# Optimization experiments

Hardware: AMD Instinct MI355X
Metric: run time of the kernel (lower is better)

## Reference

```python
import jax, jax.numpy as jnp
import numpy as np

N_ORDER = 256
BATCH = 512
SEQ_LEN = 4096


def make_legs_matrices(N):
    # HiPPO-LegS: A[n,k] = -sqrt(2n+1)sqrt(2k+1) for n>k, -(n+1) for n==k, 0 for n<k
    # B[n] = sqrt(2n+1)
    q = np.arange(N, dtype=np.float64)
    r = np.sqrt(2.0 * q + 1.0)
    M = r[:, None] * r[None, :] * (q[:, None] > q[None, :]).astype(np.float64)
    M = M + np.diag(q + 1.0)
    A = -M
    B = r[:, None]
    return jnp.asarray(A, jnp.float32), jnp.asarray(B, jnp.float32)


def setup_inputs() -> dict:
    key = jax.random.key(0)
    A, Bm = make_legs_matrices(N_ORDER)
    f = jax.random.normal(key, (BATCH, SEQ_LEN), dtype=jnp.float32)
    init_state = jnp.zeros((BATCH, 1, N_ORDER), dtype=jnp.float32)
    return {"f": f, "A": A, "Bm": Bm, "init_state": init_state}


def reference(f, A, Bm, init_state):
    # Generalized bilinear transform discretization, alpha = 0.5, step = 1.0
    step = 1.0
    alpha = 0.5
    N = A.shape[0]
    I = jnp.eye(N, dtype=A.dtype)
    inv_step = 1.0 / step
    part1 = I - inv_step * alpha * A
    part2 = I + inv_step * (1.0 - alpha) * A
    # Original uses lstsq; part1 is nonsingular so solve is equivalent.
    Ad = jnp.linalg.solve(part1, part2)            # (N, N)
    Bd = jnp.linalg.solve(part1, inv_step * Bm)    # (N, 1)

    BdT = Bd.T[None]  # (1, 1, N)

    def step_fn(c, f_k):
        # c: (B, 1, N), f_k: (B,)
        # c_k = c_{k-1} @ Ad^T + Bd^T * f_k
        c = jnp.einsum('bin,mn->bim', c, Ad) + BdT * f_k[:, None, None]
        return c, None

    # scan over time axis; batch fully vectorized inside each step
    c_k, _ = jax.lax.scan(step_fn, init_state, jnp.swapaxes(f, 0, 1))
    return c_k  # (B, 1, N)
```

## Files before the change

### kernel.cpp

```cpp
#include <hip/hip_runtime.h>

#define NORD 256
#define TLEN 4096
#define HTLEN 2048
#define NBATCH 512


__device__ __forceinline__ void tile_fma4(const float (*As)[68], const float (*Bs)[68],
                                          int tr, int tc, float acc[4][4]) {
#pragma unroll
  for (int k = 0; k < 32; ++k) {
    const float4 a4 = *reinterpret_cast<const float4*>(&As[k][4 * tr]);
    const float4 b4 = *reinterpret_cast<const float4*>(&Bs[k][4 * tc]);
    const float a[4] = {a4.x, a4.y, a4.z, a4.w};
    const float b[4] = {b4.x, b4.y, b4.z, b4.w};
#pragma unroll
    for (int ii = 0; ii < 4; ++ii)
#pragma unroll
      for (int jj = 0; jj < 4; ++jj)
        acc[ii][jj] += a[ii] * b[jj];
  }
}

__device__ __forceinline__ void fill_tr(float (*dst)[68], const float* __restrict__ s0,
                                        const float* __restrict__ s1,
                                        int row0, int stride, int k0, int t) {
  const int rr = t >> 3, cc = (t & 7) << 2;
#pragma unroll
  for (int p = 0; p < 64; p += 32) {
    const size_t off = (size_t)(row0 + rr + p) * stride + k0 + cc;
    float4 v = *reinterpret_cast<const float4*>(s0 + off);
    if (s1) {
      const float4 w = *reinterpret_cast<const float4*>(s1 + off);
      v.x += w.x; v.y += w.y; v.z += w.z; v.w += w.w;
    }
    dst[cc + 0][rr + p] = v.x; dst[cc + 1][rr + p] = v.y;
    dst[cc + 2][rr + p] = v.z; dst[cc + 3][rr + p] = v.w;
  }
}

__global__ __launch_bounds__(256) void k_inv(const float* __restrict__ A,
                                             const float* __restrict__ Bm,
                                             float* __restrict__ P00, float* P01,
                                             float* __restrict__ U0, float* U1) {
  const int bid = blockIdx.x;
  const int i = threadIdx.x;
  const int wave = i >> 6, lane = i & 63;
  __shared__ float xs[NORD];
  float b = (bid < NORD) ? ((i == bid) ? 1.0f : 0.0f) : Bm[i];
  const float invd = 1.0f / (1.0f - 0.5f * A[i * NORD + i]);
  for (int w = 0; w < 4; ++w) {
    if (wave == w) {
      const int base = w << 6;
      for (int jj = 0; jj < 64; ++jj) {
        float bj = __shfl(b, jj);
        float dj = __shfl(invd, jj);
        float xj = bj * dj;
        if (lane > jj) {
          b += 0.5f * A[i * NORD + base + jj] * xj;
        } else if (lane == jj) {
          b = xj;
        }
      }
      xs[i] = b;
    }
    __syncthreads();
    if (wave > w) {
      const int base = w << 6;
      const float4* arow = reinterpret_cast<const float4*>(A + i * NORD + base);
#pragma unroll
      for (int q = 0; q < 16; ++q) {
        float4 a4 = arow[q];
        b += 0.5f * (a4.x * xs[base + 4 * q + 0] + a4.y * xs[base + 4 * q + 1] +
                     a4.z * xs[base + 4 * q + 2] + a4.w * xs[base + 4 * q + 3]);
      }
    }
  }
  if (bid < NORD) {
    P00[i * NORD + bid] = 2.0f * b - ((i == bid) ? 1.0f : 0.0f);
    if (P01) P01[(size_t)bid * 256 + i] = 0.0f;
  } else {
    U0[i] = b;
    if (U1) U1[i] = 0.0f;
  }
}

__global__ __launch_bounds__(256) void k_stage(float* U0, float* U1,
                                               const float* Pin0, const float* Pin1,
                                               float* Pout0, float* Pout1,
                                               int J, int n_apply) {
  const int bid = blockIdx.x;
  const int t = threadIdx.x;
  const int tr = t >> 4, tc = t & 15;
  __shared__ float As[32][68];
  __shared__ float Bs[32][68];
  const int kspan = U1 ? 128 : 256;

  if (bid < n_apply) {
    int work = bid, ks = 0;
    if (U1) { ks = work & 1; work >>= 1; }
    const int j0 = (work >> 2) << 6;
    const int m0 = (work & 3) << 6;
    const int klo = ks * kspan;
    float acc[4][4] = {};
    for (int kc = 0; kc < kspan; kc += 32) {
      const int k0 = klo + kc;
      fill_tr(As, U0, U1, j0, NORD, k0, t);
      fill_tr(Bs, Pin0, Pin1, m0, NORD, k0, t);
      __syncthreads();
      tile_fma4(As, Bs, tr, tc, acc);
      __syncthreads();
    }
    float* Ud = ks ? U1 : U0;
#pragma unroll
    for (int ii = 0; ii < 4; ++ii) {
      const int lr = j0 + 4 * tr + ii;
      if (lr < J) {
        float4 v = {acc[ii][0], acc[ii][1], acc[ii][2], acc[ii][3]};
        *reinterpret_cast<float4*>(&Ud[(size_t)(J + lr) * NORD + m0 + 4 * tc]) = v;
      }
    }
  } else {
    int q = bid - n_apply, ks = 0;
    if (Pin1) { ks = q & 1; q >>= 1; }
    const int m0s = (q >> 2) << 6;
    const int n0 = (q & 3) << 6;
    const int klo = ks * kspan;
    const int rr = t >> 3, cc = (t & 7) << 2;
    float acc[4][4] = {};
    for (int kc = 0; kc < kspan; kc += 32) {
      const int k0 = klo + kc;
      fill_tr(As, Pin0, Pin1, m0s, NORD, k0, t);
#pragma unroll
      for (int p = 0; p < 64; p += 32) {
        const size_t off = (size_t)(k0 + rr) * NORD + n0 + cc + p;
        float4 v = *reinterpret_cast<const float4*>(Pin0 + off);
        if (Pin1) {
          const float4 w = *reinterpret_cast<const float4*>(Pin1 + off);
          v.x += w.x; v.y += w.y; v.z += w.z; v.w += w.w;
        }
        *reinterpret_cast<float4*>(&Bs[rr][cc + p]) = v;
      }
      __syncthreads();
      tile_fma4(As, Bs, tr, tc, acc);
      __syncthreads();
    }
    float* Pd = ks ? Pout1 : Pout0;
#pragma unroll
    for (int ii = 0; ii < 4; ++ii) {
      float4 v = {acc[ii][0], acc[ii][1], acc[ii][2], acc[ii][3]};
      *reinterpret_cast<float4*>(&Pd[(size_t)(m0s + 4 * tr + ii) * NORD + n0 + 4 * tc]) = v;
    }
  }
}

__global__ __launch_bounds__(256) void k_final(const float* __restrict__ f,
                                               const float* __restrict__ U0,
                                               const float* U1,
                                               float* __restrict__ Glow,
                                               float* __restrict__ C) {
  const int bid = blockIdx.x;
  const int tile = bid & 31, ksf = bid >> 5;
  const int rt = tile >> 1, ct = tile & 1;
  const int h = rt >> 3;
  const int b0 = (rt & 7) << 6;
  const int m0 = ct << 7;
  const int jbase = ksf << 7;
  const int t = threadIdx.x;
  const int tr = t >> 4, tc = t & 15;
  __shared__ float As[32][68];
  __shared__ float Bs0[32][68];
  __shared__ float Bs1[32][68];
  const int rr = t >> 3, cc = (t & 7) << 2;
  const int jr = t >> 5, c32 = t & 31;
  float acc[4][8] = {};
  for (int kc = 0; kc < 128; kc += 32) {
    const int j0 = jbase + kc;
#pragma unroll
    for (int p = 0; p < 64; p += 32) {
      const float4 v = *reinterpret_cast<const float4*>(
          f + (size_t)(b0 + rr + p) * TLEN + HTLEN * h + j0 + cc);
      As[cc + 0][rr + p] = v.x; As[cc + 1][rr + p] = v.y;
      As[cc + 2][rr + p] = v.z; As[cc + 3][rr + p] = v.w;
    }
#pragma unroll
    for (int p = 0; p < 32; p += 8) {
      const int jj = jr + p;
      const size_t off = (size_t)(HTLEN - 1 - (j0 + jj)) * NORD + m0 + 4 * c32;
      float4 v = *reinterpret_cast<const float4*>(U0 + off);
      if (U1) {
        const float4 w = *reinterpret_cast<const float4*>(U1 + off);
        v.x += w.x; v.y += w.y; v.z += w.z; v.w += w.w;
      }
      if (c32 < 16) *reinterpret_cast<float4*>(&Bs0[jj][4 * c32]) = v;
      else          *reinterpret_cast<float4*>(&Bs1[jj][4 * (c32 - 16)]) = v;
    }
    __syncthreads();
#pragma unroll
    for (int k = 0; k < 32; ++k) {
      const float4 a4 = *reinterpret_cast<const float4*>(&As[k][4 * tr]);
      const float4 b4 = *reinterpret_cast<const float4*>(&Bs0[k][4 * tc]);
      const float4 b5 = *reinterpret_cast<const float4*>(&Bs1[k][4 * tc]);
      const float a[4] = {a4.x, a4.y, a4.z, a4.w};
      const float b[8] = {b4.x, b4.y, b4.z, b4.w, b5.x, b5.y, b5.z, b5.w};
#pragma unroll
      for (int ii = 0; ii < 4; ++ii)
#pragma unroll
        for (int jj = 0; jj < 8; ++jj)
          acc[ii][jj] += a[ii] * b[jj];
    }
    __syncthreads();
  }
  float* dst = h ? C : Glow;
#pragma unroll
  for (int ii = 0; ii < 4; ++ii) {
    const int row = b0 + 4 * tr + ii;
#pragma unroll
    for (int jj = 0; jj < 8; ++jj) {
      const int col = m0 + ((jj < 4) ? (4 * tc + jj) : (64 + 4 * tc + (jj - 4)));
      atomicAdd(dst + (size_t)row * NORD + col, acc[ii][jj]);
    }
  }
}

__global__ __launch_bounds__(256) void k_combine(const float* __restrict__ Glow,
                                                 const float* __restrict__ P0,
                                                 const float* P1,
                                                 float* __restrict__ C) {
  const int bid = blockIdx.x;
  const int b0 = (bid >> 2) << 6;
  const int m0 = (bid & 3) << 6;
  const int t = threadIdx.x;
  const int tr = t >> 4, tc = t & 15;
  __shared__ float As[32][68];
  __shared__ float Bs[32][68];
  float acc[4][4] = {};
  for (int k0 = 0; k0 < NORD; k0 += 32) {
    fill_tr(As, Glow, nullptr, b0, NORD, k0, t);
    fill_tr(Bs, P0, P1, m0, NORD, k0, t);
    __syncthreads();
    tile_fma4(As, Bs, tr, tc, acc);
    __syncthreads();
  }
#pragma unroll
  for (int ii = 0; ii < 4; ++ii)
#pragma unroll
    for (int jj = 0; jj < 4; ++jj) {
      float* p = C + (size_t)(b0 + 4 * tr + ii) * NORD + m0 + 4 * tc + jj;
      *p += acc[ii][jj];
    }
}

extern "C" void kernel_launch(void* const* d_in, const int* in_sizes, int n_in,
                              void* d_out, int out_size, void* d_ws, size_t ws_size,
                              hipStream_t stream) {
  const float* f  = (const float*)d_in[0];
  const float* A  = (const float*)d_in[1];
  const float* Bm = (const float*)d_in[2];

  float* ws = (float*)d_ws;
  const size_t need_split = (size_t)(4 * 65536 + 2 * 524288 + 131072) * sizeof(float);
  const int KS = (ws_size >= need_split) ? 2 : 1;

  float *P00, *P01, *P10, *P11, *U0, *U1, *Glow;
  if (KS == 2) {
    P00 = ws;            P01 = ws + 65536;
    P10 = ws + 131072;   P11 = ws + 196608;
    U0  = ws + 262144;   U1  = U0 + 524288;
    Glow = U0 + 1048576;
  } else {
    P00 = ws;            P01 = nullptr;
    P10 = ws + 65536;    P11 = nullptr;
    U0  = ws + 131072;   U1  = nullptr;
    Glow = ws + 655360;
  }
  float* C = (float*)d_out;

  hipMemsetAsync(d_out, 0, (size_t)NBATCH * NORD * sizeof(float), stream);
  hipMemsetAsync(Glow, 0, (size_t)NBATCH * NORD * sizeof(float), stream);

  hipLaunchKernelGGL(k_inv, dim3(NORD + 1), dim3(256), 0, stream, A, Bm, P00, P01, U0, U1);

  for (int s = 0; s <= 10; ++s) {
    const int J = 1 << s;
    const float* Pin0 = (s & 1) ? P10 : P00;
    const float* Pin1 = (s & 1) ? P11 : P01;
    float* Pout0 = (s & 1) ? P00 : P10;
    float* Pout1 = (s & 1) ? P01 : P11;
    const int rtiles = (J + 63) >> 6;
    const int n_apply = (rtiles << 2) * KS;
    const int n_sq = 16 * KS;
    hipLaunchKernelGGL(k_stage, dim3(n_apply + n_sq), dim3(256), 0, stream,
                       U0, U1, Pin0, Pin1, Pout0, Pout1, J, n_apply);
  }

  hipLaunchKernelGGL(k_final, dim3(512), dim3(256), 0, stream, f, U0, U1, Glow, C);
  hipLaunchKernelGGL(k_combine, dim3(32), dim3(256), 0, stream, Glow, P10, P11, C);
}
```

Before: 259.9 us.

## Fuse all stages into one cooperative persistent kernel with hierarchical grid barrier

Replaces the separate inverse, eleven doubling-stage, final and combine launches plus two memsets with a single cooperative kernel of 256 blocks. Phases are separated by a two-level atomic grid barrier, and the memsets are folded into phase 0. The final phase is re-tiled so each block covers a 256-long time chunk instead of 128. The goal is to remove per-launch overhead and idle gaps between the many small launches. In exchange every block pays barrier latency at each phase, and most blocks sit idle during the small stages.

Measured after the change: 456.4 us. +75.6%, slower.

```diff
diff --git a/kernel.cpp b/kernel.cpp
--- a/kernel.cpp
+++ b/kernel.cpp
@@ -4,7 +4,36 @@
 #define TLEN 4096
 #define HTLEN 2048
 #define NBATCH 512
-
+#define NBLK 256
+#define NTHR 256
+
+__device__ __forceinline__ void gbar(int* bar) {
+  __syncthreads();
+  if (threadIdx.x == 0) {
+    int* gen = bar;
+    int* root = bar + 32;
+    int* grpc = bar + 64 + ((blockIdx.x >> 4) << 5);
+    const int g = __hip_atomic_load(gen, __ATOMIC_RELAXED, __HIP_MEMORY_SCOPE_AGENT);
+    __threadfence();
+    bool last = false;
+    if (__hip_atomic_fetch_add(grpc, 1, __ATOMIC_ACQ_REL, __HIP_MEMORY_SCOPE_AGENT) ==
+        (g << 4) + 15) {
+      if (__hip_atomic_fetch_add(root, 1, __ATOMIC_ACQ_REL, __HIP_MEMORY_SCOPE_AGENT) ==
+          (g << 4) + 15) {
+        __hip_atomic_store(gen, g + 1, __ATOMIC_RELEASE, __HIP_MEMORY_SCOPE_AGENT);
+        last = true;
+      }
+    }
+    if (!last) {
+      for (int spin = 0; spin < (1 << 22); ++spin) {
+        if (__hip_atomic_load(gen, __ATOMIC_RELAXED, __HIP_MEMORY_SCOPE_AGENT) != g) break;
+        __builtin_amdgcn_s_sleep(2);
+      }
+    }
+    __threadfence();
+  }
+  __syncthreads();
+}
 
 __device__ __forceinline__ void tile_fma4(const float (*As)[68], const float (*Bs)[68],
                                           int tr, int tc, float acc[4][4]) {
@@ -39,216 +68,227 @@
   }
 }
 
-__global__ __launch_bounds__(256) void k_inv(const float* __restrict__ A,
-                                             const float* __restrict__ Bm,
-                                             float* __restrict__ P00, float* P01,
-                                             float* __restrict__ U0, float* U1) {
-  const int bid = blockIdx.x;
-  const int i = threadIdx.x;
-  const int wave = i >> 6, lane = i & 63;
-  __shared__ float xs[NORD];
-  float b = (bid < NORD) ? ((i == bid) ? 1.0f : 0.0f) : Bm[i];
-  const float invd = 1.0f / (1.0f - 0.5f * A[i * NORD + i]);
-  for (int w = 0; w < 4; ++w) {
-    if (wave == w) {
-      const int base = w << 6;
-      for (int jj = 0; jj < 64; ++jj) {
-        float bj = __shfl(b, jj);
-        float dj = __shfl(invd, jj);
-        float xj = bj * dj;
-        if (lane > jj) {
-          b += 0.5f * A[i * NORD + base + jj] * xj;
-        } else if (lane == jj) {
-          b = xj;
-        }
-      }
-      xs[i] = b;
-    }
-    __syncthreads();
-    if (wave > w) {
-      const int base = w << 6;
-      const float4* arow = reinterpret_cast<const float4*>(A + i * NORD + base);
-#pragma unroll
-      for (int q = 0; q < 16; ++q) {
-        float4 a4 = arow[q];
-        b += 0.5f * (a4.x * xs[base + 4 * q + 0] + a4.y * xs[base + 4 * q + 1] +
-                     a4.z * xs[base + 4 * q + 2] + a4.w * xs[base + 4 * q + 3]);
-      }
-    }
-  }
-  if (bid < NORD) {
-    P00[i * NORD + bid] = 2.0f * b - ((i == bid) ? 1.0f : 0.0f);
-    if (P01) P01[(size_t)bid * 256 + i] = 0.0f;
-  } else {
-    U0[i] = b;
-    if (U1) U1[i] = 0.0f;
-  }
-}
-
-__global__ __launch_bounds__(256) void k_stage(float* U0, float* U1,
-                                               const float* Pin0, const float* Pin1,
-                                               float* Pout0, float* Pout1,
-                                               int J, int n_apply) {
+__global__ __launch_bounds__(NTHR) void hippo_all(
+    const float* __restrict__ A, const float* __restrict__ Bm,
+    const float* __restrict__ f,
+    float* P00, float* P01, float* P10, float* P11,
+    float* U0, float* U1, float* Glow, float* C,
+    int* bar, int ph_lo, int ph_hi, int use_bar) {
   const int bid = blockIdx.x;
   const int t = threadIdx.x;
   const int tr = t >> 4, tc = t & 15;
-  __shared__ float As[32][68];
-  __shared__ float Bs[32][68];
-  const int kspan = U1 ? 128 : 256;
-
-  if (bid < n_apply) {
-    int work = bid, ks = 0;
-    if (U1) { ks = work & 1; work >>= 1; }
-    const int j0 = (work >> 2) << 6;
-    const int m0 = (work & 3) << 6;
-    const int klo = ks * kspan;
-    float acc[4][4] = {};
-    for (int kc = 0; kc < kspan; kc += 32) {
-      const int k0 = klo + kc;
-      fill_tr(As, U0, U1, j0, NORD, k0, t);
-      fill_tr(Bs, Pin0, Pin1, m0, NORD, k0, t);
-      __syncthreads();
-      tile_fma4(As, Bs, tr, tc, acc);
-      __syncthreads();
-    }
-    float* Ud = ks ? U1 : U0;
-#pragma unroll
-    for (int ii = 0; ii < 4; ++ii) {
-      const int lr = j0 + 4 * tr + ii;
-      if (lr < J) {
-        float4 v = {acc[ii][0], acc[ii][1], acc[ii][2], acc[ii][3]};
-        *reinterpret_cast<float4*>(&Ud[(size_t)(J + lr) * NORD + m0 + 4 * tc]) = v;
-      }
-    }
-  } else {
-    int q = bid - n_apply, ks = 0;
-    if (Pin1) { ks = q & 1; q >>= 1; }
-    const int m0s = (q >> 2) << 6;
-    const int n0 = (q & 3) << 6;
-    const int klo = ks * kspan;
-    const int rr = t >> 3, cc = (t & 7) << 2;
-    float acc[4][4] = {};
-    for (int kc = 0; kc < kspan; kc += 32) {
-      const int k0 = klo + kc;
-      fill_tr(As, Pin0, Pin1, m0s, NORD, k0, t);
-#pragma unroll
-      for (int p = 0; p < 64; p += 32) {
-        const size_t off = (size_t)(k0 + rr) * NORD + n0 + cc + p;
-        float4 v = *reinterpret_cast<const float4*>(Pin0 + off);
-        if (Pin1) {
-          const float4 w = *reinterpret_cast<const float4*>(Pin1 + off);
-          v.x += w.x; v.y += w.y; v.z += w.z; v.w += w.w;
-        }
-        *reinterpret_cast<float4*>(&Bs[rr][cc + p]) = v;
-      }
-      __syncthreads();
-      tile_fma4(As, Bs, tr, tc, acc);
-      __syncthreads();
-    }
-    float* Pd = ks ? Pout1 : Pout0;
-#pragma unroll
-    for (int ii = 0; ii < 4; ++ii) {
-      float4 v = {acc[ii][0], acc[ii][1], acc[ii][2], acc[ii][3]};
-      *reinterpret_cast<float4*>(&Pd[(size_t)(m0s + 4 * tr + ii) * NORD + n0 + 4 * tc]) = v;
-    }
-  }
-}
-
-__global__ __launch_bounds__(256) void k_final(const float* __restrict__ f,
-                                               const float* __restrict__ U0,
-                                               const float* U1,
-                                               float* __restrict__ Glow,
-                                               float* __restrict__ C) {
-  const int bid = blockIdx.x;
-  const int tile = bid & 31, ksf = bid >> 5;
-  const int rt = tile >> 1, ct = tile & 1;
-  const int h = rt >> 3;
-  const int b0 = (rt & 7) << 6;
-  const int m0 = ct << 7;
-  const int jbase = ksf << 7;
-  const int t = threadIdx.x;
-  const int tr = t >> 4, tc = t & 15;
+
+  __shared__ float xs[NORD];
   __shared__ float As[32][68];
   __shared__ float Bs0[32][68];
   __shared__ float Bs1[32][68];
-  const int rr = t >> 3, cc = (t & 7) << 2;
-  const int jr = t >> 5, c32 = t & 31;
-  float acc[4][8] = {};
-  for (int kc = 0; kc < 128; kc += 32) {
-    const int j0 = jbase + kc;
-#pragma unroll
-    for (int p = 0; p < 64; p += 32) {
-      const float4 v = *reinterpret_cast<const float4*>(
-          f + (size_t)(b0 + rr + p) * TLEN + HTLEN * h + j0 + cc);
-      As[cc + 0][rr + p] = v.x; As[cc + 1][rr + p] = v.y;
-      As[cc + 2][rr + p] = v.z; As[cc + 3][rr + p] = v.w;
-    }
-#pragma unroll
-    for (int p = 0; p < 32; p += 8) {
-      const int jj = jr + p;
-      const size_t off = (size_t)(HTLEN - 1 - (j0 + jj)) * NORD + m0 + 4 * c32;
-      float4 v = *reinterpret_cast<const float4*>(U0 + off);
-      if (U1) {
-        const float4 w = *reinterpret_cast<const float4*>(U1 + off);
-        v.x += w.x; v.y += w.y; v.z += w.z; v.w += w.w;
-      }
-      if (c32 < 16) *reinterpret_cast<float4*>(&Bs0[jj][4 * c32]) = v;
-      else          *reinterpret_cast<float4*>(&Bs1[jj][4 * (c32 - 16)]) = v;
-    }
-    __syncthreads();
-#pragma unroll
-    for (int k = 0; k < 32; ++k) {
-      const float4 a4 = *reinterpret_cast<const float4*>(&As[k][4 * tr]);
-      const float4 b4 = *reinterpret_cast<const float4*>(&Bs0[k][4 * tc]);
-      const float4 b5 = *reinterpret_cast<const float4*>(&Bs1[k][4 * tc]);
-      const float a[4] = {a4.x, a4.y, a4.z, a4.w};
-      const float b[8] = {b4.x, b4.y, b4.z, b4.w, b5.x, b5.y, b5.z, b5.w};
+
+  for (int ph = ph_lo; ph <= ph_hi; ++ph) {
+    if (ph == 0) {
+      {
+        const int base = bid * 512;
+        C[base + t] = 0.0f; C[base + 256 + t] = 0.0f;
+        Glow[base + t] = 0.0f; Glow[base + 256 + t] = 0.0f;
+        if (P01) P01[(size_t)bid * 256 + t] = 0.0f;
+        if (U1 && bid == 0) U1[t] = 0.0f;
+      }
+      const int ntask = (bid == 0) ? 2 : 1;
+      for (int task = 0; task < ntask; ++task) {
+        const int col = (task == 0) ? (NORD - 1 - bid) : -1;
+        const int i = t;
+        const int wave = i >> 6, lane = i & 63;
+        float b = (col >= 0) ? ((i == col) ? 1.0f : 0.0f) : Bm[i];
+        const float invd = 1.0f / (1.0f - 0.5f * A[i * NORD + i]);
+        for (int w = 0; w < 4; ++w) {
+          if (wave == w) {
+            const int base = w << 6;
+            for (int jj = 0; jj < 64; ++jj) {
+              float bj = __shfl(b, jj);
+              float dj = __shfl(invd, jj);
+              float xj = bj * dj;
+              if (lane > jj) {
+                b += 0.5f * A[i * NORD + base + jj] * xj;
+              } else if (lane == jj) {
+                b = xj;
+              }
+            }
+            xs[i] = b;
+          }
+          __syncthreads();
+          if (wave > w) {
+            const int base = w << 6;
+            const float4* arow = reinterpret_cast<const float4*>(A + i * NORD + base);
+#pragma unroll
+            for (int q = 0; q < 16; ++q) {
+              float4 a4 = arow[q];
+              b += 0.5f * (a4.x * xs[base + 4 * q + 0] + a4.y * xs[base + 4 * q + 1] +
+                           a4.z * xs[base + 4 * q + 2] + a4.w * xs[base + 4 * q + 3]);
+            }
+          }
+        }
+        if (col >= 0) {
+          P00[i * NORD + col] = 2.0f * b - ((i == col) ? 1.0f : 0.0f);
+        } else {
+          U0[i] = b;
+        }
+        __syncthreads();
+      }
+    } else if (ph <= 11) {
+      const int s = ph - 1;
+      const int J = 1 << s;
+      const float* Pin0 = (s & 1) ? P10 : P00;
+      const float* Pin1 = (s & 1) ? P11 : P01;
+      float* Pout0 = (s & 1) ? P00 : P10;
+      float* Pout1 = (s & 1) ? P01 : P11;
+      const int KS = U1 ? 2 : 1;
+      const int rtiles = (J + 63) >> 6;
+      const int n_apply = (rtiles << 2) * KS;
+      const int kspan = U1 ? 128 : 256;
+
+      if (bid < n_apply) {
+        int work = bid, ks = 0;
+        if (U1) { ks = work & 1; work >>= 1; }
+        const int j0 = (work >> 2) << 6;
+        const int m0 = (work & 3) << 6;
+        const int klo = ks * kspan;
+        float acc[4][4] = {};
+        for (int kc = 0; kc < kspan; kc += 32) {
+          const int k0 = klo + kc;
+          fill_tr(As, U0, U1, j0, NORD, k0, t);
+          fill_tr(Bs0, Pin0, Pin1, m0, NORD, k0, t);
+          __syncthreads();
+          tile_fma4(As, Bs0, tr, tc, acc);
+          __syncthreads();
+        }
+        float* Ud = ks ? U1 : U0;
+#pragma unroll
+        for (int ii = 0; ii < 4; ++ii) {
+          const int lr = j0 + 4 * tr + ii;
+          if (lr < J) {
+            float4 v = {acc[ii][0], acc[ii][1], acc[ii][2], acc[ii][3]};
+            *reinterpret_cast<float4*>(&Ud[(size_t)(J + lr) * NORD + m0 + 4 * tc]) = v;
+          }
+        }
+      } else if (bid < n_apply + 16 * KS) {
+        int q = bid - n_apply, ks = 0;
+        if (Pin1) { ks = q & 1; q >>= 1; }
+        const int m0s = (q >> 2) << 6;
+        const int n0 = (q & 3) << 6;
+        const int klo = ks * kspan;
+        const int rr = t >> 3, cc = (t & 7) << 2;
+        float acc[4][4] = {};
+        for (int kc = 0; kc < kspan; kc += 32) {
+          const int k0 = klo + kc;
+          fill_tr(As, Pin0, Pin1, m0s, NORD, k0, t);
+#pragma unroll
+          for (int p = 0; p < 64; p += 32) {
+            const size_t off = (size_t)(k0 + rr) * NORD + n0 + cc + p;
+            float4 v = *reinterpret_cast<const float4*>(Pin0 + off);
+            if (Pin1) {
+              const float4 w = *reinterpret_cast<const float4*>(Pin1 + off);
+              v.x += w.x; v.y += w.y; v.z += w.z; v.w += w.w;
+            }
+            *reinterpret_cast<float4*>(&Bs0[rr][cc + p]) = v;
+          }
+          __syncthreads();
+          tile_fma4(As, Bs0, tr, tc, acc);
+          __syncthreads();
+        }
+        float* Pd = ks ? Pout1 : Pout0;
+#pragma unroll
+        for (int ii = 0; ii < 4; ++ii) {
+          float4 v = {acc[ii][0], acc[ii][1], acc[ii][2], acc[ii][3]};
+          *reinterpret_cast<float4*>(&Pd[(size_t)(m0s + 4 * tr + ii) * NORD + n0 + 4 * tc]) = v;
+        }
+      }
+    } else if (ph == 12) {
+      const int tile = bid >> 3, ks = bid & 7;
+      const int rt = tile >> 1, ct = tile & 1;
+      const int h = rt >> 3;
+      const int b0 = (rt & 7) << 6;
+      const int m0 = ct << 7;
+      const int jbase = ks << 8;
+      const int rr = t >> 3, cc = (t & 7) << 2;
+      const int jr = t >> 5, c32 = t & 31;
+      float acc[4][8] = {};
+      for (int kc = 0; kc < 256; kc += 32) {
+        const int j0 = jbase + kc;
+#pragma unroll
+        for (int p = 0; p < 64; p += 32) {
+          const float4 v = *reinterpret_cast<const float4*>(
+              f + (size_t)(b0 + rr + p) * TLEN + HTLEN * h + j0 + cc);
+          As[cc + 0][rr + p] = v.x; As[cc + 1][rr + p] = v.y;
+          As[cc + 2][rr + p] = v.z; As[cc + 3][rr + p] = v.w;
+        }
+#pragma unroll
+        for (int p = 0; p < 32; p += 8) {
+          const int jj = jr + p;
+          const size_t off = (size_t)(HTLEN - 1 - (j0 + jj)) * NORD + m0 + 4 * c32;
+          float4 v = *reinterpret_cast<const float4*>(U0 + off);
+          if (U1) {
+            const float4 w = *reinterpret_cast<const float4*>(U1 + off);
+            v.x += w.x; v.y += w.y; v.z += w.z; v.w += w.w;
+          }
+          if (c32 < 16) *reinterpret_cast<float4*>(&Bs0[jj][4 * c32]) = v;
+          else          *reinterpret_cast<float4*>(&Bs1[jj][4 * (c32 - 16)]) = v;
+        }
+        __syncthreads();
+#pragma unroll
+        for (int k = 0; k < 32; ++k) {
+          const float4 a4 = *reinterpret_cast<const float4*>(&As[k][4 * tr]);
+          const float4 b4 = *reinterpret_cast<const float4*>(&Bs0[k][4 * tc]);
+          const float4 b5 = *reinterpret_cast<const float4*>(&Bs1[k][4 * tc]);
+          const float a[4] = {a4.x, a4.y, a4.z, a4.w};
+          const float b[8] = {b4.x, b4.y, b4.z, b4.w, b5.x, b5.y, b5.z, b5.w};
+#pragma unroll
+          for (int ii = 0; ii < 4; ++ii)
+#pragma unroll
+            for (int jj = 0; jj < 8; ++jj)
+              acc[ii][jj] += a[ii] * b[jj];
+        }
+        __syncthreads();
+      }
+      float* dst = h ? C : Glow;
+#pragma unroll
+      for (int ii = 0; ii < 4; ++ii) {
+        const int row = b0 + 4 * tr + ii;
+#pragma unroll
+        for (int jj = 0; jj < 8; ++jj) {
+          const int col = m0 + ((jj < 4) ? (4 * tc + jj) : (64 + 4 * tc + (jj - 4)));
+          atomicAdd(dst + (size_t)row * NORD + col, acc[ii][jj]);
+        }
+      }
+    } else if (bid < 32) {
+      const int b0 = (bid >> 2) << 6;
+      const int m0 = (bid & 3) << 6;
+      const int rr = t >> 3, cc = (t & 7) << 2;
+      float acc[4][4] = {};
+      for (int k0 = 0; k0 < NORD; k0 += 32) {
+#pragma unroll
+        for (int p = 0; p < 64; p += 32) {
+          const size_t off = (size_t)(b0 + rr + p) * NORD + k0 + cc;
+#pragma unroll
+          for (int q = 0; q < 4; ++q)
+            As[cc + q][rr + p] =
+                __hip_atomic_load(Glow + off + q, __ATOMIC_RELAXED, __HIP_MEMORY_SCOPE_AGENT);
+        }
+        fill_tr(Bs0, P10, P11, m0, NORD, k0, t);
+        __syncthreads();
+        tile_fma4(As, Bs0, tr, tc, acc);
+        __syncthreads();
+      }
 #pragma unroll
       for (int ii = 0; ii < 4; ++ii)
 #pragma unroll
-        for (int jj = 0; jj < 8; ++jj)
-          acc[ii][jj] += a[ii] * b[jj];
-    }
-    __syncthreads();
-  }
-  float* dst = h ? C : Glow;
-#pragma unroll
-  for (int ii = 0; ii < 4; ++ii) {
-    const int row = b0 + 4 * tr + ii;
-#pragma unroll
-    for (int jj = 0; jj < 8; ++jj) {
-      const int col = m0 + ((jj < 4) ? (4 * tc + jj) : (64 + 4 * tc + (jj - 4)));
-      atomicAdd(dst + (size_t)row * NORD + col, acc[ii][jj]);
-    }
-  }
-}
-
-__global__ __launch_bounds__(256) void k_combine(const float* __restrict__ Glow,
-                                                 const float* __restrict__ P0,
-                                                 const float* P1,
-                                                 float* __restrict__ C) {
-  const int bid = blockIdx.x;
-  const int b0 = (bid >> 2) << 6;
-  const int m0 = (bid & 3) << 6;
-  const int t = threadIdx.x;
-  const int tr = t >> 4, tc = t & 15;
-  __shared__ float As[32][68];
-  __shared__ float Bs[32][68];
-  float acc[4][4] = {};
-  for (int k0 = 0; k0 < NORD; k0 += 32) {
-    fill_tr(As, Glow, nullptr, b0, NORD, k0, t);
-    fill_tr(Bs, P0, P1, m0, NORD, k0, t);
-    __syncthreads();
-    tile_fma4(As, Bs, tr, tc, acc);
-    __syncthreads();
-  }
-#pragma unroll
-  for (int ii = 0; ii < 4; ++ii)
-#pragma unroll
-    for (int jj = 0; jj < 4; ++jj) {
-      float* p = C + (size_t)(b0 + 4 * tr + ii) * NORD + m0 + 4 * tc + jj;
-      *p += acc[ii][jj];
-    }
+        for (int jj = 0; jj < 4; ++jj) {
+          float* p = C + (size_t)(b0 + 4 * tr + ii) * NORD + m0 + 4 * tc + jj;
+          const float cur =
+              __hip_atomic_load(p, __ATOMIC_RELAXED, __HIP_MEMORY_SCOPE_AGENT);
+          *p = cur + acc[ii][jj];
+        }
+    }
+    if (use_bar && ph < ph_hi) gbar(bar);
+  }
 }
 
 extern "C" void kernel_launch(void* const* d_in, const int* in_sizes, int n_in,
@@ -259,41 +299,41 @@
   const float* Bm = (const float*)d_in[2];
 
   float* ws = (float*)d_ws;
-  const size_t need_split = (size_t)(4 * 65536 + 2 * 524288 + 131072) * sizeof(float);
+  const size_t need_split =
+      (size_t)(4 * 65536 + 2 * 524288 + 131072 + 1024) * sizeof(float);
   const int KS = (ws_size >= need_split) ? 2 : 1;
 
   float *P00, *P01, *P10, *P11, *U0, *U1, *Glow;
+  int* bar;
   if (KS == 2) {
     P00 = ws;            P01 = ws + 65536;
     P10 = ws + 131072;   P11 = ws + 196608;
-    U0  = ws + 262144;   U1  = U0 + 524288;
-    Glow = U0 + 1048576;
+    U0  = ws + 262144;   U1  = ws + 786432;
+    Glow = ws + 1310720;
+    bar = (int*)(ws + 1441792);
   } else {
     P00 = ws;            P01 = nullptr;
     P10 = ws + 65536;    P11 = nullptr;
     U0  = ws + 131072;   U1  = nullptr;
     Glow = ws + 655360;
+    bar = (int*)(ws + 786432);
   }
   float* C = (float*)d_out;
 
-  hipMemsetAsync(d_out, 0, (size_t)NBATCH * NORD * sizeof(float), stream);
-  hipMemsetAsync(Glow, 0, (size_t)NBATCH * NORD * sizeof(float), stream);
-
-  hipLaunchKernelGGL(k_inv, dim3(NORD + 1), dim3(256), 0, stream, A, Bm, P00, P01, U0, U1);
-
-  for (int s = 0; s <= 10; ++s) {
-    const int J = 1 << s;
-    const float* Pin0 = (s & 1) ? P10 : P00;
-    const float* Pin1 = (s & 1) ? P11 : P01;
-    float* Pout0 = (s & 1) ? P00 : P10;
-    float* Pout1 = (s & 1) ? P01 : P11;
-    const int rtiles = (J + 63) >> 6;
-    const int n_apply = (rtiles << 2) * KS;
-    const int n_sq = 16 * KS;
-    hipLaunchKernelGGL(k_stage, dim3(n_apply + n_sq), dim3(256), 0, stream,
-                       U0, U1, Pin0, Pin1, Pout0, Pout1, J, n_apply);
-  }
-
-  hipLaunchKernelGGL(k_final, dim3(512), dim3(256), 0, stream, f, U0, U1, Glow, C);
-  hipLaunchKernelGGL(k_combine, dim3(32), dim3(256), 0, stream, Glow, P10, P11, C);
-}
+  hipMemsetAsync(bar, 0, 576 * sizeof(int), stream);
+
+  int pl = 0, phh = 13, ub = 1;
+  void* args[] = {(void*)&A, (void*)&Bm, (void*)&f,
+                  (void*)&P00, (void*)&P01, (void*)&P10, (void*)&P11,
+                  (void*)&U0, (void*)&U1, (void*)&Glow, (void*)&C,
+                  (void*)&bar, (void*)&pl, (void*)&phh, (void*)&ub};
+  hipError_t e = hipLaunchCooperativeKernel((void*)hippo_all, dim3(NBLK), dim3(NTHR),
+                                            args, 0, stream);
+  if (e != hipSuccess) {
+    for (int p = 0; p <= 13; ++p) {
+      hipLaunchKernelGGL(hippo_all, dim3(NBLK), dim3(NTHR), 0, stream,
+                         A, Bm, f, P00, P01, P10, P11, U0, U1, Glow, C,
+                         bar, p, p, 0);
+    }
+  }
+}
```

## Extend impulse-response table to full sequence and drop combine pass

Applied to the files above, without the earlier changes.

Runs one more doubling stage so the Krylov table U covers all 4096 timesteps instead of half. The final state then comes from a single GEMM of f against the reversed U, and the two-half Glow buffer and the k_combine multiply by P are removed. The output zeroing moves into k_inv, replacing the two memsets, and k_final is retiled to 32 batch rows by 256 columns. In exchange, the extra stage doubles U generation work and its memory footprint, and the final GEMM reads twice as much U data.

Result: faster. 246.4 us (-5.2%).

```diff
diff --git a/kernel.cpp b/kernel.cpp
--- a/kernel.cpp
+++ b/kernel.cpp
@@ -2,9 +2,7 @@
 
 #define NORD 256
 #define TLEN 4096
-#define HTLEN 2048
 #define NBATCH 512
-
 
 __device__ __forceinline__ void tile_fma4(const float (*As)[68], const float (*Bs)[68],
                                           int tr, int tc, float acc[4][4]) {
@@ -42,11 +40,17 @@
 __global__ __launch_bounds__(256) void k_inv(const float* __restrict__ A,
                                              const float* __restrict__ Bm,
                                              float* __restrict__ P00, float* P01,
-                                             float* __restrict__ U0, float* U1) {
+                                             float* __restrict__ U0, float* U1,
+                                             float* __restrict__ C) {
   const int bid = blockIdx.x;
   const int i = threadIdx.x;
   const int wave = i >> 6, lane = i & 63;
   __shared__ float xs[NORD];
+  if (bid < NORD) {
+    const int base = bid * 512;
+    C[base + i] = 0.0f;
+    C[base + 256 + i] = 0.0f;
+  }
   float b = (bid < NORD) ? ((i == bid) ? 1.0f : 0.0f) : Bm[i];
   const float invd = 1.0f / (1.0f - 0.5f * A[i * NORD + i]);
   for (int w = 0; w < 4; ++w) {
@@ -157,98 +161,63 @@
 __global__ __launch_bounds__(256) void k_final(const float* __restrict__ f,
                                                const float* __restrict__ U0,
                                                const float* U1,
-                                               float* __restrict__ Glow,
                                                float* __restrict__ C) {
   const int bid = blockIdx.x;
-  const int tile = bid & 31, ksf = bid >> 5;
-  const int rt = tile >> 1, ct = tile & 1;
-  const int h = rt >> 3;
-  const int b0 = (rt & 7) << 6;
-  const int m0 = ct << 7;
-  const int jbase = ksf << 7;
+  const int bt = bid >> 5;
+  const int ks = bid & 31;
+  const int b0 = bt << 5;
   const int t = threadIdx.x;
   const int tr = t >> 4, tc = t & 15;
-  __shared__ float As[32][68];
-  __shared__ float Bs0[32][68];
-  __shared__ float Bs1[32][68];
-  const int rr = t >> 3, cc = (t & 7) << 2;
-  const int jr = t >> 5, c32 = t & 31;
-  float acc[4][8] = {};
-  for (int kc = 0; kc < 128; kc += 32) {
-    const int j0 = jbase + kc;
-#pragma unroll
-    for (int p = 0; p < 64; p += 32) {
+  __shared__ float As[32][36];
+  __shared__ float Bs[32][260];
+  float acc[2][16] = {};
+  for (int ch = 0; ch < 4; ++ch) {
+    const int k0 = (ks << 7) + (ch << 5);
+    {
+      const int rr = t >> 3, cc = (t & 7) << 2;
       const float4 v = *reinterpret_cast<const float4*>(
-          f + (size_t)(b0 + rr + p) * TLEN + HTLEN * h + j0 + cc);
-      As[cc + 0][rr + p] = v.x; As[cc + 1][rr + p] = v.y;
-      As[cc + 2][rr + p] = v.z; As[cc + 3][rr + p] = v.w;
-    }
-#pragma unroll
-    for (int p = 0; p < 32; p += 8) {
-      const int jj = jr + p;
-      const size_t off = (size_t)(HTLEN - 1 - (j0 + jj)) * NORD + m0 + 4 * c32;
-      float4 v = *reinterpret_cast<const float4*>(U0 + off);
-      if (U1) {
-        const float4 w = *reinterpret_cast<const float4*>(U1 + off);
-        v.x += w.x; v.y += w.y; v.z += w.z; v.w += w.w;
-      }
-      if (c32 < 16) *reinterpret_cast<float4*>(&Bs0[jj][4 * c32]) = v;
-      else          *reinterpret_cast<float4*>(&Bs1[jj][4 * (c32 - 16)]) = v;
+          f + (size_t)(b0 + rr) * TLEN + k0 + cc);
+      As[cc + 0][rr] = v.x; As[cc + 1][rr] = v.y;
+      As[cc + 2][rr] = v.z; As[cc + 3][rr] = v.w;
+    }
+    {
+      const int kk = t >> 6, c4 = (t & 63) << 2;
+#pragma unroll
+      for (int p = 0; p < 8; ++p) {
+        const int row = (p << 2) + kk;
+        const size_t off = (size_t)(TLEN - 1 - (k0 + row)) * NORD + c4;
+        float4 v = *reinterpret_cast<const float4*>(U0 + off);
+        if (U1) {
+          const float4 w = *reinterpret_cast<const float4*>(U1 + off);
+          v.x += w.x; v.y += w.y; v.z += w.z; v.w += w.w;
+        }
+        *reinterpret_cast<float4*>(&Bs[row][c4]) = v;
+      }
     }
     __syncthreads();
 #pragma unroll
     for (int k = 0; k < 32; ++k) {
-      const float4 a4 = *reinterpret_cast<const float4*>(&As[k][4 * tr]);
-      const float4 b4 = *reinterpret_cast<const float4*>(&Bs0[k][4 * tc]);
-      const float4 b5 = *reinterpret_cast<const float4*>(&Bs1[k][4 * tc]);
-      const float a[4] = {a4.x, a4.y, a4.z, a4.w};
-      const float b[8] = {b4.x, b4.y, b4.z, b4.w, b5.x, b5.y, b5.z, b5.w};
-#pragma unroll
-      for (int ii = 0; ii < 4; ++ii)
-#pragma unroll
-        for (int jj = 0; jj < 8; ++jj)
-          acc[ii][jj] += a[ii] * b[jj];
+      const float2 a2 = *reinterpret_cast<const float2*>(&As[k][2 * tr]);
+#pragma unroll
+      for (int j = 0; j < 4; ++j) {
+        const float4 b4 = *reinterpret_cast<const float4*>(&Bs[k][(j << 6) + 4 * tc]);
+        acc[0][4 * j + 0] += a2.x * b4.x; acc[0][4 * j + 1] += a2.x * b4.y;
+        acc[0][4 * j + 2] += a2.x * b4.z; acc[0][4 * j + 3] += a2.x * b4.w;
+        acc[1][4 * j + 0] += a2.y * b4.x; acc[1][4 * j + 1] += a2.y * b4.y;
+        acc[1][4 * j + 2] += a2.y * b4.z; acc[1][4 * j + 3] += a2.y * b4.w;
+      }
     }
     __syncthreads();
   }
-  float* dst = h ? C : Glow;
-#pragma unroll
-  for (int ii = 0; ii < 4; ++ii) {
-    const int row = b0 + 4 * tr + ii;
-#pragma unroll
-    for (int jj = 0; jj < 8; ++jj) {
-      const int col = m0 + ((jj < 4) ? (4 * tc + jj) : (64 + 4 * tc + (jj - 4)));
-      atomicAdd(dst + (size_t)row * NORD + col, acc[ii][jj]);
-    }
-  }
-}
-
-__global__ __launch_bounds__(256) void k_combine(const float* __restrict__ Glow,
-                                                 const float* __restrict__ P0,
-                                                 const float* P1,
-                                                 float* __restrict__ C) {
-  const int bid = blockIdx.x;
-  const int b0 = (bid >> 2) << 6;
-  const int m0 = (bid & 3) << 6;
-  const int t = threadIdx.x;
-  const int tr = t >> 4, tc = t & 15;
-  __shared__ float As[32][68];
-  __shared__ float Bs[32][68];
-  float acc[4][4] = {};
-  for (int k0 = 0; k0 < NORD; k0 += 32) {
-    fill_tr(As, Glow, nullptr, b0, NORD, k0, t);
-    fill_tr(Bs, P0, P1, m0, NORD, k0, t);
-    __syncthreads();
-    tile_fma4(As, Bs, tr, tc, acc);
-    __syncthreads();
-  }
-#pragma unroll
-  for (int ii = 0; ii < 4; ++ii)
-#pragma unroll
-    for (int jj = 0; jj < 4; ++jj) {
-      float* p = C + (size_t)(b0 + 4 * tr + ii) * NORD + m0 + 4 * tc + jj;
-      *p += acc[ii][jj];
-    }
+#pragma unroll
+  for (int i = 0; i < 2; ++i) {
+    const size_t rowoff = (size_t)(b0 + 2 * tr + i) * NORD;
+#pragma unroll
+    for (int j = 0; j < 4; ++j)
+#pragma unroll
+      for (int q = 0; q < 4; ++q)
+        atomicAdd(&C[rowoff + (j << 6) + 4 * tc + q], acc[i][4 * j + q]);
+  }
 }
 
 extern "C" void kernel_launch(void* const* d_in, const int* in_sizes, int n_in,
@@ -259,29 +228,25 @@
   const float* Bm = (const float*)d_in[2];
 
   float* ws = (float*)d_ws;
-  const size_t need_split = (size_t)(4 * 65536 + 2 * 524288 + 131072) * sizeof(float);
+  const size_t need_split = (size_t)(4 * 65536 + 2 * 1048576) * sizeof(float);
   const int KS = (ws_size >= need_split) ? 2 : 1;
 
-  float *P00, *P01, *P10, *P11, *U0, *U1, *Glow;
+  float *P00, *P01, *P10, *P11, *U0, *U1;
   if (KS == 2) {
     P00 = ws;            P01 = ws + 65536;
     P10 = ws + 131072;   P11 = ws + 196608;
-    U0  = ws + 262144;   U1  = U0 + 524288;
-    Glow = U0 + 1048576;
+    U0  = ws + 262144;   U1  = ws + 1310720;
   } else {
     P00 = ws;            P01 = nullptr;
     P10 = ws + 65536;    P11 = nullptr;
     U0  = ws + 131072;   U1  = nullptr;
-    Glow = ws + 655360;
   }
   float* C = (float*)d_out;
 
-  hipMemsetAsync(d_out, 0, (size_t)NBATCH * NORD * sizeof(float), stream);
-  hipMemsetAsync(Glow, 0, (size_t)NBATCH * NORD * sizeof(float), stream);
-
-  hipLaunchKernelGGL(k_inv, dim3(NORD + 1), dim3(256), 0, stream, A, Bm, P00, P01, U0, U1);
-
-  for (int s = 0; s <= 10; ++s) {
+  hipLaunchKernelGGL(k_inv, dim3(NORD + 1), dim3(256), 0, stream,
+                     A, Bm, P00, P01, U0, U1, C);
+
+  for (int s = 0; s <= 11; ++s) {
     const int J = 1 << s;
     const float* Pin0 = (s & 1) ? P10 : P00;
     const float* Pin1 = (s & 1) ? P11 : P01;
@@ -289,11 +254,10 @@
     float* Pout1 = (s & 1) ? P01 : P11;
     const int rtiles = (J + 63) >> 6;
     const int n_apply = (rtiles << 2) * KS;
-    const int n_sq = 16 * KS;
+    const int n_sq = (s < 11) ? 16 * KS : 0;
     hipLaunchKernelGGL(k_stage, dim3(n_apply + n_sq), dim3(256), 0, stream,
                        U0, U1, Pin0, Pin1, Pout0, Pout1, J, n_apply);
   }
 
-  hipLaunchKernelGGL(k_final, dim3(512), dim3(256), 0, stream, f, U0, U1, Glow, C);
-  hipLaunchKernelGGL(k_combine, dim3(32), dim3(256), 0, stream, Glow, P10, P11, C);
-}
+  hipLaunchKernelGGL(k_final, dim3(512), dim3(256), 0, stream, f, U0, U1, C);
+}
```

## Compute full-length impulse response, seed doubling with direct powers, reduce split-K partials

Applied to the files above, without the earlier changes.

Replaces the half-length impulse response plus combine-with-Ad^2048 scheme with a full 4096-step impulse response table, so the final stage is a single GEMM over the full sequence and the k_combine GEMM disappears. A new k_pow kernel computes Ad^32 and the first 32 response vectors by repeated matrix-vector products, skipping the first five doubling stages. The final GEMM writes per-split partials to workspace, and a separate reduce kernel sums them instead of using atomics. The output zeroing moves into k_inv, dropping the memsets. In exchange, the response table doubles in size, more workspace is needed, and k_pow runs 32 serial steps inside only 65 blocks.

After: 384.1 us. +47.8%, slower.

```diff
diff --git a/kernel.cpp b/kernel.cpp
--- a/kernel.cpp
+++ b/kernel.cpp
@@ -2,9 +2,7 @@
 
 #define NORD 256
 #define TLEN 4096
-#define HTLEN 2048
 #define NBATCH 512
-
 
 __device__ __forceinline__ void tile_fma4(const float (*As)[68], const float (*Bs)[68],
                                           int tr, int tc, float acc[4][4]) {
@@ -42,11 +40,17 @@
 __global__ __launch_bounds__(256) void k_inv(const float* __restrict__ A,
                                              const float* __restrict__ Bm,
                                              float* __restrict__ P00, float* P01,
-                                             float* __restrict__ U0, float* U1) {
+                                             float* __restrict__ U0, float* U1,
+                                             float* __restrict__ C) {
   const int bid = blockIdx.x;
   const int i = threadIdx.x;
   const int wave = i >> 6, lane = i & 63;
   __shared__ float xs[NORD];
+  if (bid < NORD) {
+    const int base = bid * 512;
+    C[base + i] = 0.0f;
+    C[base + 256 + i] = 0.0f;
+  }
   float b = (bid < NORD) ? ((i == bid) ? 1.0f : 0.0f) : Bm[i];
   const float invd = 1.0f / (1.0f - 0.5f * A[i * NORD + i]);
   for (int w = 0; w < 4; ++w) {
@@ -85,6 +89,66 @@
   }
 }
 
+__global__ __launch_bounds__(256) void k_pow(const float* __restrict__ Ad,
+                                             float* __restrict__ P10, float* P11,
+                                             float* __restrict__ U0, float* U1) {
+  const int bid = blockIdx.x;
+  const int r = threadIdx.x;
+  __shared__ float Xs[NORD][4];
+
+  if (bid < 64) {
+    const int c0 = bid << 2;
+    float4 x;
+    x.x = (r == c0 + 0) ? 1.0f : 0.0f;
+    x.y = (r == c0 + 1) ? 1.0f : 0.0f;
+    x.z = (r == c0 + 2) ? 1.0f : 0.0f;
+    x.w = (r == c0 + 3) ? 1.0f : 0.0f;
+    for (int step = 0; step < 32; ++step) {
+      *reinterpret_cast<float4*>(&Xs[r][0]) = x;
+      __syncthreads();
+      float4 a = {0.0f, 0.0f, 0.0f, 0.0f};
+      const float4* arow = reinterpret_cast<const float4*>(Ad + (size_t)r * NORD);
+#pragma unroll 8
+      for (int k4 = 0; k4 < 64; ++k4) {
+        const float4 ad = arow[k4];
+        const float4 x0 = *reinterpret_cast<const float4*>(&Xs[4 * k4 + 0][0]);
+        const float4 x1 = *reinterpret_cast<const float4*>(&Xs[4 * k4 + 1][0]);
+        const float4 x2 = *reinterpret_cast<const float4*>(&Xs[4 * k4 + 2][0]);
+        const float4 x3 = *reinterpret_cast<const float4*>(&Xs[4 * k4 + 3][0]);
+        a.x += ad.x * x0.x + ad.y * x1.x + ad.z * x2.x + ad.w * x3.x;
+        a.y += ad.x * x0.y + ad.y * x1.y + ad.z * x2.y + ad.w * x3.y;
+        a.z += ad.x * x0.z + ad.y * x1.z + ad.z * x2.z + ad.w * x3.z;
+        a.w += ad.x * x0.w + ad.y * x1.w + ad.z * x2.w + ad.w * x3.w;
+      }
+      x = a;
+      __syncthreads();
+    }
+    *reinterpret_cast<float4*>(&P10[(size_t)r * NORD + c0]) = x;
+    if (P11) {
+      const float4 z = {0.0f, 0.0f, 0.0f, 0.0f};
+      *reinterpret_cast<float4*>(&P11[(size_t)r * NORD + c0]) = z;
+    }
+  } else {
+    float x = U0[r];
+    for (int j = 1; j < 32; ++j) {
+      Xs[r][0] = x;
+      __syncthreads();
+      float a = 0.0f;
+      const float4* arow = reinterpret_cast<const float4*>(Ad + (size_t)r * NORD);
+#pragma unroll 8
+      for (int k4 = 0; k4 < 64; ++k4) {
+        const float4 ad = arow[k4];
+        a += ad.x * Xs[4 * k4 + 0][0] + ad.y * Xs[4 * k4 + 1][0] +
+             ad.z * Xs[4 * k4 + 2][0] + ad.w * Xs[4 * k4 + 3][0];
+      }
+      U0[(size_t)j * NORD + r] = a;
+      if (U1) U1[(size_t)j * NORD + r] = 0.0f;
+      x = a;
+      __syncthreads();
+    }
+  }
+}
+
 __global__ __launch_bounds__(256) void k_stage(float* U0, float* U1,
                                                const float* Pin0, const float* Pin1,
                                                float* Pout0, float* Pout1,
@@ -157,15 +221,13 @@
 __global__ __launch_bounds__(256) void k_final(const float* __restrict__ f,
                                                const float* __restrict__ U0,
                                                const float* U1,
-                                               float* __restrict__ Glow,
+                                               float* __restrict__ Pp,
                                                float* __restrict__ C) {
   const int bid = blockIdx.x;
-  const int tile = bid & 31, ksf = bid >> 5;
-  const int rt = tile >> 1, ct = tile & 1;
-  const int h = rt >> 3;
-  const int b0 = (rt & 7) << 6;
-  const int m0 = ct << 7;
-  const int jbase = ksf << 7;
+  const int split = bid & 15;
+  const int tile = bid >> 4;
+  const int b0 = (tile >> 1) << 6;
+  const int m0 = (tile & 1) << 7;
   const int t = threadIdx.x;
   const int tr = t >> 4, tc = t & 15;
   __shared__ float As[32][68];
@@ -174,19 +236,19 @@
   const int rr = t >> 3, cc = (t & 7) << 2;
   const int jr = t >> 5, c32 = t & 31;
   float acc[4][8] = {};
-  for (int kc = 0; kc < 128; kc += 32) {
-    const int j0 = jbase + kc;
+  for (int ch = 0; ch < 8; ++ch) {
+    const int k0 = (split << 8) + (ch << 5);
 #pragma unroll
     for (int p = 0; p < 64; p += 32) {
       const float4 v = *reinterpret_cast<const float4*>(
-          f + (size_t)(b0 + rr + p) * TLEN + HTLEN * h + j0 + cc);
+          f + (size_t)(b0 + rr + p) * TLEN + k0 + cc);
       As[cc + 0][rr + p] = v.x; As[cc + 1][rr + p] = v.y;
       As[cc + 2][rr + p] = v.z; As[cc + 3][rr + p] = v.w;
     }
 #pragma unroll
     for (int p = 0; p < 32; p += 8) {
       const int jj = jr + p;
-      const size_t off = (size_t)(HTLEN - 1 - (j0 + jj)) * NORD + m0 + 4 * c32;
+      const size_t off = (size_t)(TLEN - 1 - (k0 + jj)) * NORD + m0 + 4 * c32;
       float4 v = *reinterpret_cast<const float4*>(U0 + off);
       if (U1) {
         const float4 w = *reinterpret_cast<const float4*>(U1 + off);
@@ -211,44 +273,39 @@
     }
     __syncthreads();
   }
-  float* dst = h ? C : Glow;
-#pragma unroll
-  for (int ii = 0; ii < 4; ++ii) {
-    const int row = b0 + 4 * tr + ii;
-#pragma unroll
-    for (int jj = 0; jj < 8; ++jj) {
-      const int col = m0 + ((jj < 4) ? (4 * tc + jj) : (64 + 4 * tc + (jj - 4)));
-      atomicAdd(dst + (size_t)row * NORD + col, acc[ii][jj]);
-    }
-  }
-}
-
-__global__ __launch_bounds__(256) void k_combine(const float* __restrict__ Glow,
-                                                 const float* __restrict__ P0,
-                                                 const float* P1,
-                                                 float* __restrict__ C) {
-  const int bid = blockIdx.x;
-  const int b0 = (bid >> 2) << 6;
-  const int m0 = (bid & 3) << 6;
-  const int t = threadIdx.x;
-  const int tr = t >> 4, tc = t & 15;
-  __shared__ float As[32][68];
-  __shared__ float Bs[32][68];
-  float acc[4][4] = {};
-  for (int k0 = 0; k0 < NORD; k0 += 32) {
-    fill_tr(As, Glow, nullptr, b0, NORD, k0, t);
-    fill_tr(Bs, P0, P1, m0, NORD, k0, t);
-    __syncthreads();
-    tile_fma4(As, Bs, tr, tc, acc);
-    __syncthreads();
-  }
-#pragma unroll
-  for (int ii = 0; ii < 4; ++ii)
-#pragma unroll
-    for (int jj = 0; jj < 4; ++jj) {
-      float* p = C + (size_t)(b0 + 4 * tr + ii) * NORD + m0 + 4 * tc + jj;
-      *p += acc[ii][jj];
-    }
+  if (Pp) {
+#pragma unroll
+    for (int ii = 0; ii < 4; ++ii) {
+      const size_t row = (size_t)(split * NBATCH + b0 + 4 * tr + ii) * NORD;
+      float4 v0 = {acc[ii][0], acc[ii][1], acc[ii][2], acc[ii][3]};
+      float4 v1 = {acc[ii][4], acc[ii][5], acc[ii][6], acc[ii][7]};
+      *reinterpret_cast<float4*>(&Pp[row + m0 + 4 * tc]) = v0;
+      *reinterpret_cast<float4*>(&Pp[row + m0 + 64 + 4 * tc]) = v1;
+    }
+  } else {
+#pragma unroll
+    for (int ii = 0; ii < 4; ++ii) {
+      const size_t row = (size_t)(b0 + 4 * tr + ii) * NORD;
+#pragma unroll
+      for (int jj = 0; jj < 8; ++jj) {
+        const int col = m0 + ((jj < 4) ? (4 * tc + jj) : (64 + 4 * tc + (jj - 4)));
+        atomicAdd(&C[row + col], acc[ii][jj]);
+      }
+    }
+  }
+}
+
+__global__ __launch_bounds__(256) void k_reduce(const float* __restrict__ Pp,
+                                                float* __restrict__ C) {
+  const int fi = blockIdx.x * 256 + threadIdx.x;
+  const float4* p = reinterpret_cast<const float4*>(Pp);
+  float4 s = p[fi];
+#pragma unroll
+  for (int sp = 1; sp < 16; ++sp) {
+    const float4 v = p[(size_t)sp * 32768 + fi];
+    s.x += v.x; s.y += v.y; s.z += v.z; s.w += v.w;
+  }
+  reinterpret_cast<float4*>(C)[fi] = s;
 }
 
 extern "C" void kernel_launch(void* const* d_in, const int* in_sizes, int n_in,
@@ -259,29 +316,31 @@
   const float* Bm = (const float*)d_in[2];
 
   float* ws = (float*)d_ws;
-  const size_t need_split = (size_t)(4 * 65536 + 2 * 524288 + 131072) * sizeof(float);
+  const size_t need_full  = (size_t)(4 * 65536 + 2 * 1048576 + 2097152) * sizeof(float);
+  const size_t need_split = (size_t)(4 * 65536 + 2 * 1048576) * sizeof(float);
   const int KS = (ws_size >= need_split) ? 2 : 1;
-
-  float *P00, *P01, *P10, *P11, *U0, *U1, *Glow;
+  const int has_pp = (ws_size >= need_full && KS == 2) ? 1 : 0;
+
+  float *P00, *P01, *P10, *P11, *U0, *U1, *Pp;
   if (KS == 2) {
     P00 = ws;            P01 = ws + 65536;
     P10 = ws + 131072;   P11 = ws + 196608;
-    U0  = ws + 262144;   U1  = U0 + 524288;
-    Glow = U0 + 1048576;
+    U0  = ws + 262144;   U1  = ws + 1310720;
+    Pp  = has_pp ? ws + 2359296 : nullptr;
   } else {
     P00 = ws;            P01 = nullptr;
     P10 = ws + 65536;    P11 = nullptr;
     U0  = ws + 131072;   U1  = nullptr;
-    Glow = ws + 655360;
+    Pp  = nullptr;
   }
   float* C = (float*)d_out;
 
-  hipMemsetAsync(d_out, 0, (size_t)NBATCH * NORD * sizeof(float), stream);
-  hipMemsetAsync(Glow, 0, (size_t)NBATCH * NORD * sizeof(float), stream);
-
-  hipLaunchKernelGGL(k_inv, dim3(NORD + 1), dim3(256), 0, stream, A, Bm, P00, P01, U0, U1);
-
-  for (int s = 0; s <= 10; ++s) {
+  hipLaunchKernelGGL(k_inv, dim3(NORD + 1), dim3(256), 0, stream,
+                     A, Bm, P00, P01, U0, U1, C);
+
+  hipLaunchKernelGGL(k_pow, dim3(65), dim3(256), 0, stream, P00, P10, P11, U0, U1);
+
+  for (int s = 5; s <= 11; ++s) {
     const int J = 1 << s;
     const float* Pin0 = (s & 1) ? P10 : P00;
     const float* Pin1 = (s & 1) ? P11 : P01;
@@ -289,11 +348,13 @@
     float* Pout1 = (s & 1) ? P01 : P11;
     const int rtiles = (J + 63) >> 6;
     const int n_apply = (rtiles << 2) * KS;
-    const int n_sq = 16 * KS;
+    const int n_sq = (s < 11) ? 16 * KS : 0;
     hipLaunchKernelGGL(k_stage, dim3(n_apply + n_sq), dim3(256), 0, stream,
                        U0, U1, Pin0, Pin1, Pout0, Pout1, J, n_apply);
   }
 
-  hipLaunchKernelGGL(k_final, dim3(512), dim3(256), 0, stream, f, U0, U1, Glow, C);
-  hipLaunchKernelGGL(k_combine, dim3(32), dim3(256), 0, stream, Glow, P10, P11, C);
-}
+  hipLaunchKernelGGL(k_final, dim3(256), dim3(256), 0, stream, f, U0, U1, Pp, C);
+  if (Pp) {
+    hipLaunchKernelGGL(k_reduce, dim3(128), dim3(256), 0, stream, Pp, C);
+  }
+}
```
